# Performance work log

Hardware: AMD Instinct MI355X
Metric: run time of the kernel (lower is better)

## Reference

```python
import jax, jax.numpy as jnp
import numpy as np

NUM_HEADS = 8
AGENT_NUM = 16
POOL = 4  # sqrt(agent_num)


def _block_pool(t, b, H, W, c):
    # AdaptiveAvgPool2d to (POOL, POOL); H, W divisible by POOL -> exact block mean.
    # t: (b, n, c) with n = H*W, spatial layout reshape(b, H, W, c)
    hb, wb = H // POOL, W // POOL
    t = t.reshape(b, POOL, hb, POOL, wb, c)
    return t.mean(axis=(2, 4)).reshape(b, AGENT_NUM, c)  # (b, agent_num, c)


def setup_inputs() -> dict:
    key = jax.random.key(0)
    ks = jax.random.split(key, 6)
    b, H, W, c = 32, 56, 56, 384
    n = H * W
    return {
        "x": jax.random.normal(ks[0], (b, n, c), dtype=jnp.float32),
        "H": H,
        "W": W,
        "Wq": jax.random.normal(ks[1], (c, c), dtype=jnp.float32) * 0.02,
        "Wkv": jax.random.normal(ks[2], (c, c), dtype=jnp.float32) * 0.02,
        "w_g": jax.random.normal(ks[3], (c, 1), dtype=jnp.float32) * 0.02,
        "Wp": jax.random.normal(ks[4], (c, c), dtype=jnp.float32) * 0.02,
        "bp": jax.random.normal(ks[5], (c,), dtype=jnp.float32) * 0.02,
    }


def reference(x, H, W, Wq, Wkv, w_g, Wp, bp):
    b, n, c = x.shape
    h, d = NUM_HEADS, c // NUM_HEADS
    scale = d ** -0.5

    q = x @ Wq.T            # (b, n, c)  q = Linear(x), no bias
    k = x @ Wkv.T           # (b, n, c)  kv = Linear(x), sr_ratio == 1

    agent_q = _block_pool(q, b, H, W, c)   # (b, agent_num, c)
    agent_k = _block_pool(k, b, H, W, c)   # (b, agent_num, c)

    # gating: A = (agent_q @ w_g) * scale; G = sum(A * agent_q, dim=1)
    A = (agent_q @ w_g) * scale                    # (b, agent_num, 1)
    G = jnp.sum(A * agent_q, axis=1)               # (b, c)
    agent_new = (G[:, None, :] * agent_k) @ Wp.T + bp + agent_q  # (b, agent_num, c)

    # split heads
    qh = q.reshape(b, n, h, d).transpose(0, 2, 1, 3)               # (b, h, n, d)
    an = agent_new.reshape(b, AGENT_NUM, h, d).transpose(0, 2, 1, 3)  # (b, h, a, d)
    ak = agent_k.reshape(b, AGENT_NUM, h, d).transpose(0, 2, 1, 3)    # (b, h, a, d)

    q_attn = jax.nn.softmax(jnp.einsum('bhnd,bhad->bhna', qh * scale, an), axis=-1)
    out = jnp.einsum('bhna,bhad->bhnd', q_attn, ak)                # (b, h, n, d)
    out = out.transpose(0, 2, 1, 3).reshape(b, n, c)
    return out @ Wp.T + bp  # Proj reused for output projection
```

## Files before the change

kernel.cpp:

```cpp
#include <hip/hip_runtime.h>
#include <hip/hip_bf16.h>
#include <cstdint>
#include <cstddef>

#define NB   32
#define NPOS 3136
#define NC   384
#define NHD  8
#define DH   48
#define NAG  16
#define MROWS (NB*NPOS)
#define CQK  768

static constexpr float kScale = 0.14433756729740643f;
static constexpr float kInv196 = 1.0f / 196.0f;

typedef __bf16 bf16x8 __attribute__((ext_vector_type(8)));
typedef float  f32x4  __attribute__((ext_vector_type(4)));

__global__ __launch_bounds__(256) void cvt4_kernel(const float* __restrict__ src,
                                                   __hip_bfloat16* __restrict__ dst,
                                                   int n4) {
    int i = blockIdx.x * 256 + threadIdx.x;
    if (i >= n4) return;
    float4 v = ((const float4*)src)[i];
    union { ushort4 u; __hip_bfloat16 h[4]; } p;
    p.h[0] = __float2bfloat16(v.x);
    p.h[1] = __float2bfloat16(v.y);
    p.h[2] = __float2bfloat16(v.z);
    p.h[3] = __float2bfloat16(v.w);
    ((ushort4*)dst)[i] = p.u;
}

template<bool HAS_BIAS, bool OUT_BF16, bool RESID>
__global__ __launch_bounds__(256) void gemm_kernel(
    const __hip_bfloat16* __restrict__ A,
    const __hip_bfloat16* __restrict__ Bw,
    const float* __restrict__ bias,
    const float* __restrict__ resid,
    void* __restrict__ Cout,
    int M, int Nn, int K)
{
    __shared__ unsigned char smem[16384];
    unsigned char* smA = smem;
    unsigned char* smB = smem + 8192;

    const int t    = threadIdx.x;
    const int m0   = blockIdx.x * 128;
    const int n0   = blockIdx.y * 128;
    const int lane = t & 63;
    const int wv   = t >> 6;
    const int wm   = (wv >> 1) * 64;
    const int wn   = (wv & 1) * 64;
    const int lr   = lane & 15;
    const int lg   = lane >> 4;

    const int r0 = t >> 2;
    const int c0 = t & 3;
    const int sc = (c0 ^ (r0 & 3)) << 4;

    f32x4 acc[4][4] = {};

    const int nk = K >> 5;
    for (int kt = 0; kt < nk; ++kt) {
        const int k0 = kt << 5;
        uint4 a0 = *(const uint4*)(A  + (size_t)(m0 + r0)      * K + k0 + c0 * 8);
        uint4 a1 = *(const uint4*)(A  + (size_t)(m0 + r0 + 64) * K + k0 + c0 * 8);
        uint4 b0 = *(const uint4*)(Bw + (size_t)(n0 + r0)      * K + k0 + c0 * 8);
        uint4 b1 = *(const uint4*)(Bw + (size_t)(n0 + r0 + 64) * K + k0 + c0 * 8);
        __syncthreads();
        *(uint4*)(smA + r0 * 64        + sc) = a0;
        *(uint4*)(smA + (r0 + 64) * 64 + sc) = a1;
        *(uint4*)(smB + r0 * 64        + sc) = b0;
        *(uint4*)(smB + (r0 + 64) * 64 + sc) = b1;
        __syncthreads();

        bf16x8 av[4], bv[4];
        #pragma unroll
        for (int mf = 0; mf < 4; ++mf) {
            int row = wm + mf * 16 + lr;
            av[mf] = *(const bf16x8*)(smA + row * 64 + ((lg ^ (row & 3)) << 4));
        }
        #pragma unroll
        for (int nf = 0; nf < 4; ++nf) {
            int row = wn + nf * 16 + lr;
            bv[nf] = *(const bf16x8*)(smB + row * 64 + ((lg ^ (row & 3)) << 4));
        }
        #pragma unroll
        for (int mf = 0; mf < 4; ++mf)
            #pragma unroll
            for (int nf = 0; nf < 4; ++nf)
                acc[mf][nf] = __builtin_amdgcn_mfma_f32_16x16x32_bf16(av[mf], bv[nf], acc[mf][nf], 0, 0, 0);
    }

    #pragma unroll
    for (int mf = 0; mf < 4; ++mf) {
        #pragma unroll
        for (int nf = 0; nf < 4; ++nf) {
            #pragma unroll
            for (int j = 0; j < 4; ++j) {
                int row = m0 + wm + mf * 16 + (lg << 2) + j;
                int col = n0 + wn + nf * 16 + lr;
                float v = acc[mf][nf][j];
                if (HAS_BIAS) v += bias[col];
                if (RESID)    v += resid[(size_t)row * Nn + col];
                if (OUT_BF16)
                    ((__hip_bfloat16*)Cout)[(size_t)row * Nn + col] = __float2bfloat16(v);
                else
                    ((float*)Cout)[(size_t)row * Nn + col] = v;
            }
        }
    }
}

__global__ __launch_bounds__(256) void pool_kernel(const __hip_bfloat16* __restrict__ qk,
                                                   float* __restrict__ agent_qk) {
    int idx = blockIdx.x * 256 + threadIdx.x;
    int ch4 = (idx % 192) * 4;
    int a   = (idx / 192) & 15;
    int b   = idx / 3072;
    int py = a >> 2, px = a & 3;
    const __hip_bfloat16* base = qk + (size_t)b * NPOS * CQK + ch4;
    float s0 = 0.f, s1 = 0.f, s2 = 0.f, s3 = 0.f;
    for (int dy = 0; dy < 14; ++dy) {
        int rowbase = (py * 14 + dy) * 56 + px * 14;
        #pragma unroll
        for (int dx = 0; dx < 14; ++dx) {
            union { uint2 u; __hip_bfloat16 h[4]; } v;
            v.u = *(const uint2*)(base + (size_t)(rowbase + dx) * CQK);
            s0 += (float)v.h[0];
            s1 += (float)v.h[1];
            s2 += (float)v.h[2];
            s3 += (float)v.h[3];
        }
    }
    float4 o;
    o.x = s0 * kInv196; o.y = s1 * kInv196; o.z = s2 * kInv196; o.w = s3 * kInv196;
    ((float4*)agent_qk)[idx] = o;
}

__global__ __launch_bounds__(256) void agent_prep_kernel(
    const float* __restrict__ agqk,
    const float* __restrict__ w_g,
    __hip_bfloat16* __restrict__ gkb,
    __hip_bfloat16* __restrict__ akb,
    float* __restrict__ aqf)
{
    __shared__ float aq[NAG][NC];
    __shared__ float Av[NAG];
    __shared__ float G[NC];
    const int b = blockIdx.x, t = threadIdx.x;
    const float* base = agqk + (size_t)b * NAG * CQK;

    for (int i = t; i < NAG * NC; i += 256) {
        int a = i / NC, cc = i - a * NC;
        aq[a][cc] = base[a * CQK + cc];
    }
    __syncthreads();

    {
        int a = t >> 4, l = t & 15;
        float s = 0.f;
        for (int cc = l; cc < NC; cc += 16) s += aq[a][cc] * w_g[cc];
        s += __shfl_down(s, 8, 16);
        s += __shfl_down(s, 4, 16);
        s += __shfl_down(s, 2, 16);
        s += __shfl_down(s, 1, 16);
        if (l == 0) Av[a] = s * kScale;
    }
    __syncthreads();

    for (int cc = t; cc < NC; cc += 256) {
        float s = 0.f;
        #pragma unroll
        for (int a = 0; a < NAG; ++a) s += Av[a] * aq[a][cc];
        G[cc] = s;
    }
    __syncthreads();

    for (int i = t; i < NAG * NC; i += 256) {
        int a = i / NC, cc = i - a * NC;
        float kv = base[a * CQK + NC + cc];
        size_t o = (size_t)b * NAG * NC + i;
        akb[o] = __float2bfloat16(kv);
        gkb[o] = __float2bfloat16(G[cc] * kv);
        aqf[o] = aq[a][cc];
    }
}

__global__ __launch_bounds__(256) void attn_kernel(
    const __hip_bfloat16* __restrict__ qk,
    const __hip_bfloat16* __restrict__ anb,
    const __hip_bfloat16* __restrict__ akb,
    __hip_bfloat16* __restrict__ outb)
{
    const int bh = blockIdx.x;
    const int b = bh >> 3, hd = bh & 7;
    __shared__ float an_s[NAG][DH];
    __shared__ float ak_s[NAG][DH];
    const int t = threadIdx.x;
    for (int i = t; i < NAG * DH; i += 256) {
        int a = i / DH, dd = i - a * DH;
        an_s[a][dd] = (float)anb[((size_t)b * NAG + a) * NC + hd * DH + dd];
        ak_s[a][dd] = (float)akb[((size_t)b * NAG + a) * NC + hd * DH + dd];
    }
    __syncthreads();
    const int row = blockIdx.y * 256 + t;
    if (row >= NPOS) return;

    union { uint4 u[6]; __hip_bfloat16 h[48]; } qv;
    const uint4* qp = (const uint4*)(qk + ((size_t)b * NPOS + row) * CQK + hd * DH);
    #pragma unroll
    for (int i = 0; i < 6; ++i) qv.u[i] = qp[i];
    float qf[DH];
    #pragma unroll
    for (int dd = 0; dd < DH; ++dd) qf[dd] = (float)qv.h[dd];

    float sv[NAG];
    float mx = -1e30f;
    #pragma unroll
    for (int a = 0; a < NAG; ++a) {
        float s = 0.f;
        #pragma unroll
        for (int dd = 0; dd < DH; ++dd) s += qf[dd] * an_s[a][dd];
        s *= kScale;
        sv[a] = s;
        mx = fmaxf(mx, s);
    }
    float den = 0.f;
    #pragma unroll
    for (int a = 0; a < NAG; ++a) { sv[a] = __expf(sv[a] - mx); den += sv[a]; }
    const float inv = 1.f / den;

    float o[DH];
    #pragma unroll
    for (int dd = 0; dd < DH; ++dd) o[dd] = 0.f;
    #pragma unroll
    for (int a = 0; a < NAG; ++a) {
        float p = sv[a] * inv;
        #pragma unroll
        for (int dd = 0; dd < DH; ++dd) o[dd] += p * ak_s[a][dd];
    }

    union { uint4 u[6]; __hip_bfloat16 h[48]; } ov;
    #pragma unroll
    for (int dd = 0; dd < DH; ++dd) ov.h[dd] = __float2bfloat16(o[dd]);
    uint4* op = (uint4*)(outb + ((size_t)b * NPOS + row) * NC + hd * DH);
    #pragma unroll
    for (int i = 0; i < 6; ++i) op[i] = ov.u[i];
}

extern "C" void kernel_launch(void* const* d_in, const int* in_sizes, int n_in,
                              void* d_out, int out_size, void* d_ws, size_t ws_size,
                              hipStream_t stream) {
    (void)in_sizes; (void)n_in; (void)out_size; (void)ws_size;
    const float* x   = (const float*)d_in[0];
    const float* Wq  = (const float*)d_in[3];
    const float* Wkv = (const float*)d_in[4];
    const float* wg  = (const float*)d_in[5];
    const float* Wp  = (const float*)d_in[6];
    const float* bp  = (const float*)d_in[7];
    float* out = (float*)d_out;

    char* w = (char*)d_ws;
    __hip_bfloat16* xb   = (__hip_bfloat16*)(w);
    __hip_bfloat16* qkb  = (__hip_bfloat16*)(w + 77070336);
    __hip_bfloat16* wqkb = (__hip_bfloat16*)(w + 231211008);
    __hip_bfloat16* wpb  = (__hip_bfloat16*)(w + 231800832);
    float*          agqk = (float*)(w + 232095744);
    __hip_bfloat16* anb  = (__hip_bfloat16*)(w + 233668608);
    __hip_bfloat16* akb  = (__hip_bfloat16*)(w + 234061824);

    __hip_bfloat16* gkb = (__hip_bfloat16*)(w);
    float*          aqf = (float*)(w + 393216);

    cvt4_kernel<<<37632, 256, 0, stream>>>(x, xb, 9633792);
    cvt4_kernel<<<144, 256, 0, stream>>>(Wq,  wqkb,          36864);
    cvt4_kernel<<<144, 256, 0, stream>>>(Wkv, wqkb + 147456, 36864);
    cvt4_kernel<<<144, 256, 0, stream>>>(Wp,  wpb,           36864);

    gemm_kernel<false, true, false><<<dim3(MROWS / 128, CQK / 128), 256, 0, stream>>>(
        xb, wqkb, nullptr, nullptr, qkb, MROWS, CQK, NC);

    pool_kernel<<<384, 256, 0, stream>>>(qkb, agqk);

    agent_prep_kernel<<<NB, 256, 0, stream>>>(agqk, wg, gkb, akb, aqf);

    gemm_kernel<true, true, true><<<dim3(4, 3), 256, 0, stream>>>(
        gkb, wpb, bp, aqf, anb, NB * NAG, NC, NC);

    attn_kernel<<<dim3(NB * NHD, (NPOS + 255) / 256), 256, 0, stream>>>(qkb, anb, akb, xb);

    gemm_kernel<true, false, false><<<dim3(MROWS / 128, NC / 128), 256, 0, stream>>>(
        xb, wpb, bp, nullptr, out, MROWS, NC, NC);
}
```

Measured before the change: 545.5 us.

## Use direct global-to-LDS async loads with BK=64 and N-fastest block order in GEMM

The GEMM now stages A and B tiles through global_load_lds, which copies straight into shared memory without passing through registers. The K tile doubles to 64 with a matching 8-way XOR swizzle, halving the number of barrier pairs per tile. The 2D grid becomes 1D with the N-tile index varying fastest, so blocks sharing an A row-panel run close together and can reuse it in L2. The load is still issued between two barriers with no double buffering, so load latency is still exposed, and LDS use doubles to 32KB per block.

```diff
diff --git a/kernel.cpp b/kernel.cpp
--- a/kernel.cpp
+++ b/kernel.cpp
@@ -17,6 +17,12 @@
 
 typedef __bf16 bf16x8 __attribute__((ext_vector_type(8)));
 typedef float  f32x4  __attribute__((ext_vector_type(4)));
+
+__device__ static inline void async_copy16(void* lds, const void* g) {
+    __builtin_amdgcn_global_load_lds(
+        (const __attribute__((address_space(1))) unsigned int*)g,
+        (__attribute__((address_space(3))) unsigned int*)lds, 16, 0, 0);
+}
 
 __global__ __launch_bounds__(256) void cvt4_kernel(const float* __restrict__ src,
                                                    __hip_bfloat16* __restrict__ dst,
@@ -39,58 +45,62 @@
     const float* __restrict__ bias,
     const float* __restrict__ resid,
     void* __restrict__ Cout,
-    int M, int Nn, int K)
+    int nBlkN, int Nn, int K)
 {
-    __shared__ unsigned char smem[16384];
+    __shared__ unsigned char smem[32768];
     unsigned char* smA = smem;
-    unsigned char* smB = smem + 8192;
+    unsigned char* smB = smem + 16384;
 
     const int t    = threadIdx.x;
-    const int m0   = blockIdx.x * 128;
-    const int n0   = blockIdx.y * 128;
+    const int m0   = (blockIdx.x / nBlkN) * 128;
+    const int n0   = (blockIdx.x % nBlkN) * 128;
     const int lane = t & 63;
-    const int wv   = t >> 6;
-    const int wm   = (wv >> 1) * 64;
-    const int wn   = (wv & 1) * 64;
+    const int w    = t >> 6;
+    const int wm   = (w >> 1) * 64;
+    const int wn   = (w & 1) * 64;
     const int lr   = lane & 15;
     const int lg   = lane >> 4;
 
-    const int r0 = t >> 2;
-    const int c0 = t & 3;
-    const int sc = (c0 ^ (r0 & 3)) << 4;
+    const int Kb    = K << 1;
+    const int lrow  = lane >> 3;
+    const int lslot = ((lane & 7) ^ lrow) << 4;
+    const char* Ag = (const char*)A  + (size_t)(m0 + 32 * w + lrow) * Kb + lslot;
+    const char* Bg = (const char*)Bw + (size_t)(n0 + 32 * w + lrow) * Kb + lslot;
+    unsigned char* ldsA = smA + w * 4096;
+    unsigned char* ldsB = smB + w * 4096;
 
     f32x4 acc[4][4] = {};
 
-    const int nk = K >> 5;
+    const int nk = K >> 6;
     for (int kt = 0; kt < nk; ++kt) {
-        const int k0 = kt << 5;
-        uint4 a0 = *(const uint4*)(A  + (size_t)(m0 + r0)      * K + k0 + c0 * 8);
-        uint4 a1 = *(const uint4*)(A  + (size_t)(m0 + r0 + 64) * K + k0 + c0 * 8);
-        uint4 b0 = *(const uint4*)(Bw + (size_t)(n0 + r0)      * K + k0 + c0 * 8);
-        uint4 b1 = *(const uint4*)(Bw + (size_t)(n0 + r0 + 64) * K + k0 + c0 * 8);
         __syncthreads();
-        *(uint4*)(smA + r0 * 64        + sc) = a0;
-        *(uint4*)(smA + (r0 + 64) * 64 + sc) = a1;
-        *(uint4*)(smB + r0 * 64        + sc) = b0;
-        *(uint4*)(smB + (r0 + 64) * 64 + sc) = b1;
+        #pragma unroll
+        for (int j = 0; j < 4; ++j) {
+            async_copy16(ldsA + j * 1024, Ag + (size_t)(8 * j) * Kb);
+            async_copy16(ldsB + j * 1024, Bg + (size_t)(8 * j) * Kb);
+        }
+        Ag += 128; Bg += 128;
         __syncthreads();
 
-        bf16x8 av[4], bv[4];
-        #pragma unroll
-        for (int mf = 0; mf < 4; ++mf) {
-            int row = wm + mf * 16 + lr;
-            av[mf] = *(const bf16x8*)(smA + row * 64 + ((lg ^ (row & 3)) << 4));
+        #pragma unroll
+        for (int kk = 0; kk < 2; ++kk) {
+            bf16x8 av[4], bv[4];
+            #pragma unroll
+            for (int mf = 0; mf < 4; ++mf) {
+                const int row = wm + mf * 16 + lr;
+                av[mf] = *(const bf16x8*)(smA + row * 128 + ((((kk << 2) | lg) ^ (row & 7)) << 4));
+            }
+            #pragma unroll
+            for (int nf = 0; nf < 4; ++nf) {
+                const int row = wn + nf * 16 + lr;
+                bv[nf] = *(const bf16x8*)(smB + row * 128 + ((((kk << 2) | lg) ^ (row & 7)) << 4));
+            }
+            #pragma unroll
+            for (int mf = 0; mf < 4; ++mf)
+                #pragma unroll
+                for (int nf = 0; nf < 4; ++nf)
+                    acc[mf][nf] = __builtin_amdgcn_mfma_f32_16x16x32_bf16(av[mf], bv[nf], acc[mf][nf], 0, 0, 0);
         }
-        #pragma unroll
-        for (int nf = 0; nf < 4; ++nf) {
-            int row = wn + nf * 16 + lr;
-            bv[nf] = *(const bf16x8*)(smB + row * 64 + ((lg ^ (row & 3)) << 4));
-        }
-        #pragma unroll
-        for (int mf = 0; mf < 4; ++mf)
-            #pragma unroll
-            for (int nf = 0; nf < 4; ++nf)
-                acc[mf][nf] = __builtin_amdgcn_mfma_f32_16x16x32_bf16(av[mf], bv[nf], acc[mf][nf], 0, 0, 0);
     }
 
     #pragma unroll
@@ -279,18 +289,18 @@
     cvt4_kernel<<<144, 256, 0, stream>>>(Wkv, wqkb + 147456, 36864);
     cvt4_kernel<<<144, 256, 0, stream>>>(Wp,  wpb,           36864);
 
-    gemm_kernel<false, true, false><<<dim3(MROWS / 128, CQK / 128), 256, 0, stream>>>(
-        xb, wqkb, nullptr, nullptr, qkb, MROWS, CQK, NC);
+    gemm_kernel<false, true, false><<<(MROWS / 128) * (CQK / 128), 256, 0, stream>>>(
+        xb, wqkb, nullptr, nullptr, qkb, CQK / 128, CQK, NC);
 
     pool_kernel<<<384, 256, 0, stream>>>(qkb, agqk);
 
     agent_prep_kernel<<<NB, 256, 0, stream>>>(agqk, wg, gkb, akb, aqf);
 
-    gemm_kernel<true, true, true><<<dim3(4, 3), 256, 0, stream>>>(
-        gkb, wpb, bp, aqf, anb, NB * NAG, NC, NC);
+    gemm_kernel<true, true, true><<<4 * 3, 256, 0, stream>>>(
+        gkb, wpb, bp, aqf, anb, NC / 128, NC, NC);
 
     attn_kernel<<<dim3(NB * NHD, (NPOS + 255) / 256), 256, 0, stream>>>(qkb, anb, akb, xb);
 
-    gemm_kernel<true, false, false><<<dim3(MROWS / 128, NC / 128), 256, 0, stream>>>(
-        xb, wpb, bp, nullptr, out, MROWS, NC, NC);
-}
+    gemm_kernel<true, false, false><<<(MROWS / 128) * (NC / 128), 256, 0, stream>>>(
+        xb, wpb, bp, nullptr, out, NC / 128, NC, NC);
+}
```

Result: faster. 533.0 us (-2.3%).
